# Kernel optimization log

Hardware: AMD Instinct MI355X
Metric: run time of the kernel (lower is better)

Reference implementation:

```python
import jax, jax.numpy as jnp
import numpy as np

N_NODES = 50000
N_EDGES = 800000
N_GRAPHS = 128
IN_DIM, HID_DIM, OUT_DIM = 128, 96, 10


def setup_inputs() -> dict:
    key = jax.random.key(0)
    ks = jax.random.split(key, 9)
    x = jax.random.normal(ks[0], (N_NODES, IN_DIM), dtype=jnp.float32)
    edge_index = jax.random.randint(ks[1], (2, N_EDGES), 0, N_NODES, dtype=jnp.int32)
    batch = jnp.sort(jax.random.randint(ks[2], (N_NODES,), 0, N_GRAPHS, dtype=jnp.int32))
    s1 = 1.0 / np.sqrt(IN_DIM)
    s2 = 1.0 / np.sqrt(HID_DIM)
    W1 = jax.random.uniform(ks[3], (IN_DIM, HID_DIM), jnp.float32, -s1, s1)
    b1 = jnp.zeros((HID_DIM,), jnp.float32)
    W2 = jax.random.uniform(ks[4], (HID_DIM, HID_DIM), jnp.float32, -s2, s2)
    b2 = jnp.zeros((HID_DIM,), jnp.float32)
    Wf = jax.random.uniform(ks[5], (OUT_DIM, HID_DIM), jnp.float32, -s2, s2)
    bf = jax.random.uniform(ks[6], (OUT_DIM,), jnp.float32, -s2, s2)
    return {"x": x, "edge_index": edge_index, "batch": batch,
            "W1": W1, "b1": b1, "W2": W2, "b2": b2, "Wf": Wf, "bf": bf}


def reference(x, edge_index, batch, W1, b1, W2, b2, Wf, bf):
    n = x.shape[0]
    row, col = edge_index[0], edge_index[1]
    # GCN symmetric normalization with self-loops: deg = 1 + in-degree
    deg = jax.ops.segment_sum(jnp.ones_like(col, dtype=x.dtype), col, num_segments=n) + 1.0
    dinv = deg ** -0.5  # [N]
    norm = dinv[row] * dinv[col]  # [E]

    def gcn_conv(h, W, b):
        h = h @ W  # [N, F_out]
        # edge messages: norm_e * h[src] scattered to dst; self-loops handled analytically
        agg = jax.ops.segment_sum(norm[:, None] * h[row], col, num_segments=n)
        agg = agg + (dinv * dinv)[:, None] * h
        return agg + b

    h = jax.nn.relu(gcn_conv(x, W1, b1))
    h = gcn_conv(h, W2, b2)

    # global mean pool over graphs
    counts = jax.ops.segment_sum(jnp.ones((n,), x.dtype), batch, num_segments=N_GRAPHS)
    pooled = jax.ops.segment_sum(h, batch, num_segments=N_GRAPHS)
    pooled = pooled / jnp.maximum(counts, 1.0)[:, None]

    logits = pooled @ Wf.T + bf
    return jax.nn.log_softmax(logits, axis=1)
```

## Files before the change

kernel.cpp:

```cpp
#include <hip/hip_runtime.h>
#include <hip/hip_bf16.h>

#define N_GRAPHS 128
#define HID 96
#define OUT_DIM 10
#define CAP 64
#define TROW 128

typedef __attribute__((ext_vector_type(8))) short short8;
typedef __attribute__((ext_vector_type(4))) float f32x4;
typedef __attribute__((ext_vector_type(2))) float f32x2;

__device__ inline unsigned short f2bf(float f) {
    union { float f; unsigned u; } x;
    x.f = f;
    unsigned r = x.u + 0x7FFFu + ((x.u >> 16) & 1u);
    return (unsigned short)(r >> 16);
}

__device__ inline unsigned char f2fp8(float v) {
    int p = __builtin_amdgcn_cvt_pk_fp8_f32(v, v, 0, false);
    return (unsigned char)(p & 0xff);
}

__device__ inline void unpack16_fp8(uint4 v, float* o) {
    f32x2 a0 = __builtin_amdgcn_cvt_pk_f32_fp8((int)v.x, false);
    f32x2 a1 = __builtin_amdgcn_cvt_pk_f32_fp8((int)v.x, true);
    f32x2 b0 = __builtin_amdgcn_cvt_pk_f32_fp8((int)v.y, false);
    f32x2 b1 = __builtin_amdgcn_cvt_pk_f32_fp8((int)v.y, true);
    f32x2 c0 = __builtin_amdgcn_cvt_pk_f32_fp8((int)v.z, false);
    f32x2 c1 = __builtin_amdgcn_cvt_pk_f32_fp8((int)v.z, true);
    f32x2 d0 = __builtin_amdgcn_cvt_pk_f32_fp8((int)v.w, false);
    f32x2 d1 = __builtin_amdgcn_cvt_pk_f32_fp8((int)v.w, true);
    o[0] = a0.x;  o[1] = a0.y;  o[2] = a1.x;  o[3] = a1.y;
    o[4] = b0.x;  o[5] = b0.y;  o[6] = b1.x;  o[7] = b1.y;
    o[8] = c0.x;  o[9] = c0.y;  o[10] = c1.x; o[11] = c1.y;
    o[12] = d0.x; o[13] = d0.y; o[14] = d1.x; o[15] = d1.y;
}

__global__ __launch_bounds__(256) void fill_kernel(const int* __restrict__ rowi,
                                                   const int* __restrict__ coli,
                                                   const int* __restrict__ batch,
                                                   int* __restrict__ cnt,
                                                   int* __restrict__ gcount,
                                                   unsigned short* __restrict__ srcs,
                                                   int E, int N) {
    const int part = blockIdx.x & 7;
    const int chunk = blockIdx.x >> 3;
    const int base = chunk * 2048;
    const int plo = (int)(((long long)N * part) >> 3);
    const int phi = (int)(((long long)N * (part + 1)) >> 3);
#pragma unroll
    for (int it = 0; it < 8; ++it) {
        int e = base + it * 256 + threadIdx.x;
        if (e < E) {
            int c = coli[e];
            if (c >= plo && c < phi) {
                int pos = atomicAdd(&cnt[c], 1);
                if (pos < CAP) srcs[(size_t)c * CAP + pos] = (unsigned short)rowi[e];
            }
        }
    }
    const int gtid = blockIdx.x * 256 + threadIdx.x;
    const int nch = (N + 63) >> 6;
    if (gtid < nch) {
        const int i0 = gtid << 6;
        const int lim = min(64, N - i0);
        int gcur = batch[i0];
        int run = 0;
        for (int i = 0; i < lim; ++i) {
            int g = batch[i0 + i];
            if (g != gcur) {
                atomicAdd(&gcount[gcur], run);
                gcur = g;
                run = 0;
            }
            ++run;
        }
        atomicAdd(&gcount[gcur], run);
    }
}

__global__ __launch_bounds__(256) void gemm1_mfma(const float* __restrict__ X,
                                                  const float* __restrict__ W,
                                                  const int* __restrict__ cnt,
                                                  unsigned char* __restrict__ Tp, int N) {
    constexpr int K = 128;
    constexpr int P = K + 8;
    constexpr int KT = K / 32;
    __shared__ __align__(16) unsigned short Wt[96 * P];
    const int tid = threadIdx.x;
    const int row0 = blockIdx.x * 64;

    for (int idx = tid; idx < K * 96; idx += 256) {
        int k = idx / 96, n = idx - k * 96;
        Wt[n * P + k] = f2bf(W[idx]);
    }
    __syncthreads();

    const int wv = tid >> 6;
    const int lane = tid & 63;
    const int m = lane & 15;
    const int quad = lane >> 4;
    const int row = row0 + wv * 16 + m;

    short8 afrag[KT];
    if (row < N) {
        const float* Xr = X + (size_t)row * K;
#pragma unroll
        for (int t = 0; t < KT; ++t) {
            float4 a0 = *(const float4*)(Xr + t * 32 + quad * 8);
            float4 a1 = *(const float4*)(Xr + t * 32 + quad * 8 + 4);
            short8 a;
            a[0] = (short)f2bf(a0.x); a[1] = (short)f2bf(a0.y);
            a[2] = (short)f2bf(a0.z); a[3] = (short)f2bf(a0.w);
            a[4] = (short)f2bf(a1.x); a[5] = (short)f2bf(a1.y);
            a[6] = (short)f2bf(a1.z); a[7] = (short)f2bf(a1.w);
            afrag[t] = a;
        }
    } else {
#pragma unroll
        for (int t = 0; t < KT; ++t) afrag[t] = short8{0, 0, 0, 0, 0, 0, 0, 0};
    }

    f32x4 acc[6];
#pragma unroll
    for (int nt = 0; nt < 6; ++nt) acc[nt] = f32x4{0.f, 0.f, 0.f, 0.f};
#pragma unroll
    for (int t = 0; t < KT; ++t) {
#pragma unroll
        for (int nt = 0; nt < 6; ++nt) {
            short8 bfrag = *(const short8*)&Wt[(nt * 16 + m) * P + t * 32 + quad * 8];
            acc[nt] = __builtin_amdgcn_mfma_f32_16x16x32_bf16(afrag[t], bfrag, acc[nt], 0, 0, 0);
        }
    }
#pragma unroll
    for (int r = 0; r < 4; ++r) {
        int orow = row0 + wv * 16 + quad * 4 + r;
        if (orow < N) {
            float d = rsqrtf(1.0f + (float)cnt[orow]);
#pragma unroll
            for (int nt = 0; nt < 6; ++nt)
                Tp[(size_t)orow * TROW + nt * 16 + m] = f2fp8(d * acc[nt][r]);
        }
    }
}

__global__ __launch_bounds__(256) void gather1_gemm2(const unsigned char* __restrict__ Tp1,
                                                     const unsigned short* __restrict__ srcs,
                                                     const int* __restrict__ cnt,
                                                     const float* __restrict__ b1,
                                                     const float* __restrict__ W2,
                                                     unsigned char* __restrict__ Tp2, int N) {
    constexpr int PH = 104;
    constexpr int PW = 104;
    __shared__ __align__(16) unsigned short Hs[64 * PH];
    __shared__ __align__(16) unsigned short Wt[96 * PW];
    const int tid = threadIdx.x;
    const int node0 = blockIdx.x * 64;

    for (int idx = tid; idx < 96 * 96; idx += 256) {
        int k = idx / 96, n = idx - k * 96;
        Wt[n * PW + k] = f2bf(W2[idx]);
    }

    const uint4* Trow = (const uint4*)Tp1;
#pragma unroll
    for (int it = 0; it < 2; ++it) {
        int idx = it * 256 + tid;
        if (idx < 384) {
            int n = idx / 6, j = idx - n * 6;
            int i = node0 + n;
            if (i < N) {
                float acc[16], tmp[16];
                unpack16_fp8(Trow[((size_t)i << 3) + j], acc);
                int ci = cnt[i];
                int e = min(ci, CAP);
                const unsigned short* sp = srcs + (size_t)i * CAP;
                int k = 0;
                for (; k + 4 <= e; k += 4) {
                    ushort4 s4 = *(const ushort4*)(sp + k);
                    uint4 v0 = Trow[((size_t)s4.x << 3) + j];
                    uint4 v1 = Trow[((size_t)s4.y << 3) + j];
                    uint4 v2 = Trow[((size_t)s4.z << 3) + j];
                    uint4 v3 = Trow[((size_t)s4.w << 3) + j];
                    unpack16_fp8(v0, tmp);
#pragma unroll
                    for (int l = 0; l < 16; ++l) acc[l] += tmp[l];
                    unpack16_fp8(v1, tmp);
#pragma unroll
                    for (int l = 0; l < 16; ++l) acc[l] += tmp[l];
                    unpack16_fp8(v2, tmp);
#pragma unroll
                    for (int l = 0; l < 16; ++l) acc[l] += tmp[l];
                    unpack16_fp8(v3, tmp);
#pragma unroll
                    for (int l = 0; l < 16; ++l) acc[l] += tmp[l];
                }
                for (; k < e; ++k) {
                    unpack16_fp8(Trow[((size_t)sp[k] << 3) + j], tmp);
#pragma unroll
                    for (int l = 0; l < 16; ++l) acc[l] += tmp[l];
                }
                float di = rsqrtf(1.0f + (float)ci);
#pragma unroll
                for (int l = 0; l < 16; ++l) {
                    float v = fmaxf(di * acc[l] + b1[j * 16 + l], 0.0f);
                    Hs[n * PH + j * 16 + l] = f2bf(v);
                }
            } else {
#pragma unroll
                for (int l = 0; l < 16; ++l) Hs[n * PH + j * 16 + l] = 0;
            }
        }
    }
    __syncthreads();

    const int wv = tid >> 6;
    const int lane = tid & 63;
    const int m = lane & 15;
    const int quad = lane >> 4;
    const int lrow = wv * 16 + m;
    short8 afrag[3];
#pragma unroll
    for (int t = 0; t < 3; ++t)
        afrag[t] = *(const short8*)&Hs[lrow * PH + t * 32 + quad * 8];
    f32x4 acc[6];
#pragma unroll
    for (int nt = 0; nt < 6; ++nt) acc[nt] = f32x4{0.f, 0.f, 0.f, 0.f};
#pragma unroll
    for (int t = 0; t < 3; ++t) {
#pragma unroll
        for (int nt = 0; nt < 6; ++nt) {
            short8 bfrag = *(const short8*)&Wt[(nt * 16 + m) * PW + t * 32 + quad * 8];
            acc[nt] = __builtin_amdgcn_mfma_f32_16x16x32_bf16(afrag[t], bfrag, acc[nt], 0, 0, 0);
        }
    }
#pragma unroll
    for (int r = 0; r < 4; ++r) {
        int orow = node0 + wv * 16 + quad * 4 + r;
        if (orow < N) {
            float d = rsqrtf(1.0f + (float)cnt[orow]);
#pragma unroll
            for (int nt = 0; nt < 6; ++nt)
                Tp2[(size_t)orow * TROW + nt * 16 + m] = f2fp8(d * acc[nt][r]);
        }
    }
}

__global__ __launch_bounds__(192) void gather2_pool(const unsigned char* __restrict__ Tp,
                                                    const unsigned short* __restrict__ srcs,
                                                    const int* __restrict__ cnt,
                                                    const int* __restrict__ batch,
                                                    float* __restrict__ pooled, int N) {
    __shared__ float hl[32 * 96];
    __shared__ int g_l[32];
    const int tid = threadIdx.x;
    const int n = tid / 6;
    const int j = tid - n * 6;
    const int i = blockIdx.x * 32 + n;
    if (tid < 32) {
        int ii = blockIdx.x * 32 + tid;
        g_l[tid] = (ii < N) ? batch[ii] : -1;
    }

    float acc[16];
#pragma unroll
    for (int l = 0; l < 16; ++l) acc[l] = 0.0f;
    float di = 0.0f;
    if (i < N) {
        const uint4* Trow = (const uint4*)Tp;
        float tmp[16];
        unpack16_fp8(Trow[((size_t)i << 3) + j], acc);
        int ci = cnt[i];
        di = rsqrtf(1.0f + (float)ci);
        int e = min(ci, CAP);
        const unsigned short* sp = srcs + (size_t)i * CAP;
        int k = 0;
        for (; k + 4 <= e; k += 4) {
            ushort4 s4 = *(const ushort4*)(sp + k);
            uint4 v0 = Trow[((size_t)s4.x << 3) + j];
            uint4 v1 = Trow[((size_t)s4.y << 3) + j];
            uint4 v2 = Trow[((size_t)s4.z << 3) + j];
            uint4 v3 = Trow[((size_t)s4.w << 3) + j];
            unpack16_fp8(v0, tmp);
#pragma unroll
            for (int l = 0; l < 16; ++l) acc[l] += tmp[l];
            unpack16_fp8(v1, tmp);
#pragma unroll
            for (int l = 0; l < 16; ++l) acc[l] += tmp[l];
            unpack16_fp8(v2, tmp);
#pragma unroll
            for (int l = 0; l < 16; ++l) acc[l] += tmp[l];
            unpack16_fp8(v3, tmp);
#pragma unroll
            for (int l = 0; l < 16; ++l) acc[l] += tmp[l];
        }
        for (; k < e; ++k) {
            unpack16_fp8(Trow[((size_t)sp[k] << 3) + j], tmp);
#pragma unroll
            for (int l = 0; l < 16; ++l) acc[l] += tmp[l];
        }
    }
#pragma unroll
    for (int l = 0; l < 16; ++l) hl[n * 96 + j * 16 + l] = di * acc[l];
    __syncthreads();

    if (tid < 96) {
        int f = tid;
        float s = 0.0f;
        int gcur = -2;
        for (int nn = 0; nn < 32; ++nn) {
            int g = g_l[nn];
            if (g < 0) continue;
            if (g != gcur) {
                if (gcur >= 0) atomicAdd(&pooled[gcur * 96 + f], s);
                gcur = g;
                s = 0.0f;
            }
            s += hl[nn * 96 + f];
        }
        if (gcur >= 0) atomicAdd(&pooled[gcur * 96 + f], s);
    }
}

__global__ void head_kernel(const float* __restrict__ pooled, const int* __restrict__ gcount,
                            const float* __restrict__ b2, const float* __restrict__ Wf,
                            const float* __restrict__ bfv, float* __restrict__ out) {
    __shared__ float wfs[OUT_DIM * HID];
    __shared__ float b2s[HID];
    __shared__ float bfs[OUT_DIM];
    int t = threadIdx.x;
    for (int idx = t; idx < OUT_DIM * HID; idx += 128) wfs[idx] = Wf[idx];
    if (t < HID) b2s[t] = b2[t];
    if (t < OUT_DIM) bfs[t] = bfv[t];
    __syncthreads();
    int g = t;
    if (g >= N_GRAPHS) return;
    int c = gcount[g];
    float inv = (c > 0) ? 1.0f / (float)c : 0.0f;
    float hasb = (c > 0) ? 1.0f : 0.0f;
    float logits[OUT_DIM];
#pragma unroll
    for (int o = 0; o < OUT_DIM; ++o) {
        float s = 0.0f;
        for (int cc = 0; cc < HID; ++cc)
            s += (pooled[g * HID + cc] * inv + hasb * b2s[cc]) * wfs[o * HID + cc];
        logits[o] = s + bfs[o];
    }
    float m = logits[0];
#pragma unroll
    for (int o = 1; o < OUT_DIM; ++o) m = fmaxf(m, logits[o]);
    float se = 0.0f;
#pragma unroll
    for (int o = 0; o < OUT_DIM; ++o) se += expf(logits[o] - m);
    float lse = m + logf(se);
#pragma unroll
    for (int o = 0; o < OUT_DIM; ++o) out[g * OUT_DIM + o] = logits[o] - lse;
}

extern "C" void kernel_launch(void* const* d_in, const int* in_sizes, int n_in,
                              void* d_out, int out_size, void* d_ws, size_t ws_size,
                              hipStream_t stream) {
    const float* x     = (const float*)d_in[0];
    const int*   ei    = (const int*)d_in[1];
    const int*   batch = (const int*)d_in[2];
    const float* W1    = (const float*)d_in[3];
    const float* b1    = (const float*)d_in[4];
    const float* W2    = (const float*)d_in[5];
    const float* b2    = (const float*)d_in[6];
    const float* Wf    = (const float*)d_in[7];
    const float* bf    = (const float*)d_in[8];

    const int N = in_sizes[0] / 128;
    const int E = in_sizes[1] / 2;
    const int* rowi = ei;
    const int* coli = ei + E;

    size_t off = 0;
    auto alloc = [&](size_t bytes) {
        void* p = (char*)d_ws + off;
        off += (bytes + 255) & ~(size_t)255;
        return p;
    };
    int*            cnt    = (int*)alloc((size_t)N * 4);
    float*          pooled = (float*)alloc((size_t)N_GRAPHS * HID * 4);
    int*            gcount = (int*)alloc((size_t)N_GRAPHS * 4);
    size_t zero_bytes = off;
    unsigned short* srcs   = (unsigned short*)alloc((size_t)N * CAP * 2);
    unsigned char*  Tp1    = (unsigned char*)alloc((size_t)N * TROW);
    unsigned char*  Tp2    = (unsigned char*)alloc((size_t)N * TROW);

    hipMemsetAsync(d_ws, 0, zero_bytes, stream);

    const int nchunk = (E + 2047) / 2048;
    fill_kernel<<<nchunk * 8, 256, 0, stream>>>(rowi, coli, batch, cnt, gcount, srcs, E, N);

    gemm1_mfma<<<(N + 63) / 64, 256, 0, stream>>>(x, W1, cnt, Tp1, N);

    gather1_gemm2<<<(N + 63) / 64, 256, 0, stream>>>(Tp1, srcs, cnt, b1, W2, Tp2, N);

    gather2_pool<<<(N + 31) / 32, 192, 0, stream>>>(Tp2, srcs, cnt, batch, pooled, N);

    head_kernel<<<1, 128, 0, stream>>>(pooled, gcount, b2, Wf, bf, (float*)d_out);
}
```

Measured before the change: 210.2 us.

## Drop destination partitioning in fill kernel and vectorize edge loads

The fill kernel no longer has 8 block groups that each re-read every edge and keep only destinations in their node range. Instead each thread loads four edges with int4 loads and does the atomic slot insertion for all of them. This removes the eightfold redundant reads of the column indices and the filtering work. In exchange it gives up any locality the partitioning gave, since the blockIdx-based split probably kept each destination range on one XCD's L2, so the count and slot atomics may now be spread across the whole device.

```diff
diff --git a/kernel.cpp b/kernel.cpp
--- a/kernel.cpp
+++ b/kernel.cpp
@@ -45,26 +45,29 @@
                                                    int* __restrict__ gcount,
                                                    unsigned short* __restrict__ srcs,
                                                    int E, int N) {
-    const int part = blockIdx.x & 7;
-    const int chunk = blockIdx.x >> 3;
-    const int base = chunk * 2048;
-    const int plo = (int)(((long long)N * part) >> 3);
-    const int phi = (int)(((long long)N * (part + 1)) >> 3);
-#pragma unroll
-    for (int it = 0; it < 8; ++it) {
-        int e = base + it * 256 + threadIdx.x;
-        if (e < E) {
+    const int t = blockIdx.x * 256 + threadIdx.x;
+    const int e0 = t * 4;
+    if (e0 + 3 < E) {
+        int4 c4 = *(const int4*)(coli + e0);
+        int4 r4 = *(const int4*)(rowi + e0);
+        int p0 = atomicAdd(&cnt[c4.x], 1);
+        if (p0 < CAP) srcs[(size_t)c4.x * CAP + p0] = (unsigned short)r4.x;
+        int p1 = atomicAdd(&cnt[c4.y], 1);
+        if (p1 < CAP) srcs[(size_t)c4.y * CAP + p1] = (unsigned short)r4.y;
+        int p2 = atomicAdd(&cnt[c4.z], 1);
+        if (p2 < CAP) srcs[(size_t)c4.z * CAP + p2] = (unsigned short)r4.z;
+        int p3 = atomicAdd(&cnt[c4.w], 1);
+        if (p3 < CAP) srcs[(size_t)c4.w * CAP + p3] = (unsigned short)r4.w;
+    } else if (e0 < E) {
+        for (int e = e0; e < E; ++e) {
             int c = coli[e];
-            if (c >= plo && c < phi) {
-                int pos = atomicAdd(&cnt[c], 1);
-                if (pos < CAP) srcs[(size_t)c * CAP + pos] = (unsigned short)rowi[e];
-            }
-        }
-    }
-    const int gtid = blockIdx.x * 256 + threadIdx.x;
+            int pos = atomicAdd(&cnt[c], 1);
+            if (pos < CAP) srcs[(size_t)c * CAP + pos] = (unsigned short)rowi[e];
+        }
+    }
     const int nch = (N + 63) >> 6;
-    if (gtid < nch) {
-        const int i0 = gtid << 6;
+    if (t < nch) {
+        const int i0 = t << 6;
         const int lim = min(64, N - i0);
         int gcur = batch[i0];
         int run = 0;
@@ -393,8 +396,8 @@
 
     hipMemsetAsync(d_ws, 0, zero_bytes, stream);
 
-    const int nchunk = (E + 2047) / 2048;
-    fill_kernel<<<nchunk * 8, 256, 0, stream>>>(rowi, coli, batch, cnt, gcount, srcs, E, N);
+    const int nblk = (E / 4 + 255) / 256;
+    fill_kernel<<<nblk, 256, 0, stream>>>(rowi, coli, batch, cnt, gcount, srcs, E, N);
 
     gemm1_mfma<<<(N + 63) / 64, 256, 0, stream>>>(x, W1, cnt, Tp1, N);
 
```

Result: slower. 229.6 us (+9.3%).
